# Kernel tuning notes

Measured on AMD Instinct MI355X. Metric: run time of the kernel, lower is better.

The kernel has to match this reference:

```python
import jax, jax.numpy as jnp
import numpy as np

B, T, V, E, H, D = 2048, 50, 65, 100, 20, 5  # batch, block, vocab, n_embd, heads, head_size


def setup_inputs() -> dict:
    key = jax.random.key(0)
    ks = jax.random.split(key, 12)
    idx = jax.random.randint(ks[0], (B, T), 0, V)
    targets = jax.random.randint(ks[1], (B, T), 0, V)
    tok_emb = jax.random.normal(ks[2], (V, E), dtype=jnp.float32) * 0.02
    pos_emb = jax.random.normal(ks[3], (T, E), dtype=jnp.float32) * 0.02
    # per-head Linear(N_EMBD, head_size, bias=False) weights, stacked over heads: [H, D, E]
    Wk = jax.random.normal(ks[4], (H, D, E), dtype=jnp.float32) * 0.1
    Wq = jax.random.normal(ks[5], (H, D, E), dtype=jnp.float32) * 0.1
    Wv = jax.random.normal(ks[6], (H, D, E), dtype=jnp.float32) * 0.1
    W_ff = jax.random.normal(ks[7], (E, E), dtype=jnp.float32) * 0.1
    b_ff = jnp.zeros((E,), dtype=jnp.float32)
    W_lm = jax.random.normal(ks[8], (V, E), dtype=jnp.float32) * 0.1
    b_lm = jnp.zeros((V,), dtype=jnp.float32)
    return {"idx": idx, "targets": targets, "tok_emb": tok_emb, "pos_emb": pos_emb,
            "Wk": Wk, "Wq": Wq, "Wv": Wv, "W_ff": W_ff, "b_ff": b_ff,
            "W_lm": W_lm, "b_lm": b_lm}


def reference(idx, targets, tok_emb, pos_emb, Wk, Wq, Wv, W_ff, b_ff, W_lm, b_lm):
    Bs, Ts = idx.shape
    x = tok_emb[idx] + pos_emb[:Ts]  # [B, T, E]
    # batched over all heads (equivalent to the per-head Python loop + concat)
    k = jnp.einsum('bte,hde->bhtd', x, Wk)
    q = jnp.einsum('bte,hde->bhtd', x, Wq)
    v = jnp.einsum('bte,hde->bhtd', x, Wv)
    # NOTE: faithful to original: k @ q^T, scaled by C**0.5 (multiply, C = N_EMBD)
    scale = jnp.asarray(E, x.dtype) ** 0.5
    w = jnp.einsum('bhtd,bhsd->bhts', k, q) * scale  # [B, H, T, S]
    tril = jnp.tril(jnp.ones((Ts, Ts), dtype=bool))
    w = jnp.where(tril, w, -jnp.inf)
    # original: torch.softmax(weights, dim=1) on [B, T, S] -> axis 't' here (axis=2)
    w = jax.nn.softmax(w, axis=2)
    attn = jnp.einsum('bhts,bhsd->bhtd', w, v)
    attn = attn.transpose(0, 2, 1, 3).reshape(Bs, Ts, H * D)  # concat heads -> [B, T, E]
    h = jax.nn.relu(attn @ W_ff.T + b_ff)  # FeedForward applied AFTER attention
    logits = h @ W_lm.T + b_lm  # [B, T, V]
    logits2d = logits.reshape(Bs * Ts, V)
    tflat = targets.reshape(Bs * Ts)
    logp = jax.nn.log_softmax(logits2d, axis=-1)
    loss = -jnp.take_along_axis(logp, tflat[:, None], axis=-1).mean()
    return (logits2d, loss)
```

## Files before the change

kernel.cpp:

```cpp
#include <hip/hip_runtime.h>
#include <hip/hip_bf16.h>

#define Bb 2048
#define Tt 50
#define Vv 65
#define Ee 100
#define Hh 20
#define Dd 5

typedef __bf16 v8bf __attribute__((ext_vector_type(8)));
typedef short v8s __attribute__((ext_vector_type(8)));
typedef short v4s __attribute__((ext_vector_type(4)));
typedef float f32x4 __attribute__((ext_vector_type(4)));

__device__ __forceinline__ v8bf bzero8() {
    v8s z = {0, 0, 0, 0, 0, 0, 0, 0};
    union { v8s s; v8bf b; } u; u.s = z; return u.b;
}
__device__ __forceinline__ unsigned short bfbits(float f) {
    union { __hip_bfloat16 h; unsigned short s; } c;
    c.h = __float2bfloat16(f);
    return c.s;
}
__device__ __forceinline__ float bf2f(short s) {
    union { unsigned i; float f; } c; c.i = ((unsigned)(unsigned short)s) << 16; return c.f;
}
__device__ __forceinline__ unsigned pack2(float a, float b) {
    return (unsigned)bfbits(a) | ((unsigned)bfbits(b) << 16);
}

__device__ __forceinline__ f32x4 mfma_16x16x16_bf16(v4s a, v4s b, f32x4 c) {
#if __has_builtin(__builtin_amdgcn_mfma_f32_16x16x16bf16_1k)
    return __builtin_amdgcn_mfma_f32_16x16x16bf16_1k(a, b, c, 0, 0, 0);
#else
    f32x4 d;
    asm volatile("v_mfma_f32_16x16x16_bf16 %0, %1, %2, %3\n\ts_nop 7\n\ts_nop 4"
                 : "=v"(d) : "v"(a), "v"(b), "v"(c));
    return d;
#endif
}

#define WS_WKQV 1024
#define WS_WFF  (1024 + 81920)
#define WS_WLM  (1024 + 81920 + 32768)

#define XSTR 136
#define QLO 0
#define QHI 4000
#define KLO 5000
#define KHI 9000
#define R3V 10000
#define HST 6800
#define VSTR 52

__global__ __launch_bounds__(256) void prep_kernel(
    const float* __restrict__ Wk, const float* __restrict__ Wq,
    const float* __restrict__ Wv, const float* __restrict__ Wff,
    const float* __restrict__ Wlm, char* __restrict__ ws,
    float* __restrict__ out)
{
    int g = blockIdx.x * 256 + threadIdx.x;
    if (g == 0) out[Bb * Tt * Vv] = 0.f;
    __hip_bfloat16* wkqv = (__hip_bfloat16*)(ws + WS_WKQV);
    __hip_bfloat16* wff  = (__hip_bfloat16*)(ws + WS_WFF);
    __hip_bfloat16* wlm  = (__hip_bfloat16*)(ws + WS_WLM);
    if (g < 40960) {
        int n = g >> 7, e = g & 127;
        float v = 0.f;
        if (e < Ee) {
            if (n < 100)      v = Wk[n * Ee + e] * 14.4269504089f;
            else if (n < 200) v = Wq[(n - 100) * Ee + e];
            else if (n < 300) v = Wv[(n - 200) * Ee + e];
        }
        wkqv[g] = __float2bfloat16(v);
    } else if (g < 57344) {
        int gg = g - 40960; int n = gg >> 7, e = gg & 127;
        float v = (e < Ee && n < Ee) ? Wff[n * Ee + e] : 0.f;
        wff[gg] = __float2bfloat16(v);
    } else {
        int gg = g - 57344; int n = gg >> 7, e = gg & 127;
        float v = (e < Ee && n < Vv) ? Wlm[n * Ee + e] : 0.f;
        wlm[gg] = __float2bfloat16(v);
    }
}

__global__ __launch_bounds__(256, 4) void gpt_main(
    const int* __restrict__ idx, const int* __restrict__ targets,
    const float* __restrict__ tok_emb, const float* __restrict__ pos_emb,
    const float* __restrict__ b_ff, const float* __restrict__ b_lm,
    const char* __restrict__ ws, float* __restrict__ out)
{
    __shared__ __attribute__((aligned(16))) __hip_bfloat16 sh[15200];
    __shared__ int tok_s[Tt];
    __shared__ float bsum;

    const int b    = blockIdx.x;
    const int tid  = threadIdx.x;
    const int wave = tid >> 6;
    const int ln   = tid & 15;
    const int quad = (tid >> 4) & 3;

    if (tid < Tt) tok_s[tid] = idx[b * Tt + tid];
    if (tid == 0) bsum = 0.f;
    __syncthreads();
    for (int i = tid; i < Tt * 32; i += 256) {
        int r = i >> 5, c4 = (i & 31) * 4;
        ushort4 o;
        if (c4 < Ee) {
            const float4 te = *(const float4*)&tok_emb[tok_s[r] * Ee + c4];
            const float4 pe = *(const float4*)&pos_emb[r * Ee + c4];
            o.x = bfbits(te.x + pe.x); o.y = bfbits(te.y + pe.y);
            o.z = bfbits(te.z + pe.z); o.w = bfbits(te.w + pe.w);
        } else {
            o.x = 0; o.y = 0; o.z = 0; o.w = 0;
        }
        *(ushort4*)&sh[r * XSTR + c4] = o;
    }
    __syncthreads();

    {
        const __hip_bfloat16* wkqv = (const __hip_bfloat16*)(ws + WS_WKQV);
        f32x4 acc[5][4];
#pragma unroll
        for (int j = 0; j < 5; ++j)
#pragma unroll
            for (int mt = 0; mt < 4; ++mt) {
                f32x4 z = {0.f, 0.f, 0.f, 0.f};
                acc[j][mt] = z;
            }
#pragma unroll
        for (int kt = 0; kt < 4; ++kt) {
            v8bf a[4];
#pragma unroll
            for (int mt = 0; mt < 4; ++mt)
                a[mt] = (mt < 3 || ln < 2)
                      ? *(const v8bf*)&sh[(mt * 16 + ln) * XSTR + kt * 32 + quad * 8]
                      : bzero8();
#pragma unroll
            for (int j = 0; j < 5; ++j) {
                int nt = wave * 5 + j;
                v8bf bfr = *(const v8bf*)&wkqv[(nt * 16 + ln) * 128 + kt * 32 + quad * 8];
#pragma unroll
                for (int mt = 0; mt < 4; ++mt)
                    acc[j][mt] = __builtin_amdgcn_mfma_f32_16x16x32_bf16(a[mt], bfr, acc[j][mt], 0, 0, 0);
            }
        }
        __syncthreads();
#pragma unroll
        for (int j = 0; j < 5; ++j) {
            int n = (wave * 5 + j) * 16 + ln;
            if (n < 300) {
                int mat = n / 100;
                int jj  = n - mat * 100;
                int h   = jj / 5, d = jj - (jj / 5) * 5;
                if (mat == 2) {
                    int base = R3V + (h * 5 + d) * VSTR;
#pragma unroll
                    for (int mt = 0; mt < 4; ++mt) {
                        if (mt < 3 || quad == 0) {
                            float v0 = acc[j][mt][0], v1 = acc[j][mt][1];
                            float v2 = acc[j][mt][2], v3 = acc[j][mt][3];
                            if (mt == 3) { v2 = 0.f; v3 = 0.f; }
                            uint2 pk = make_uint2(pack2(v0, v1), pack2(v2, v3));
                            *(uint2*)&sh[base + mt * 16 + quad * 4] = pk;
                        }
                    }
                } else {
                    int lo = (mat == 0) ? KLO : QLO;
                    int hi = (mat == 0) ? KHI : QHI;
                    int rbase = h * 50;
#pragma unroll
                    for (int mt = 0; mt < 4; ++mt)
#pragma unroll
                        for (int r = 0; r < 4; ++r) {
                            int m = mt * 16 + quad * 4 + r;
                            if (m < Tt) {
                                __hip_bfloat16 val = __float2bfloat16(acc[j][mt][r]);
                                if (d < 4) sh[lo + (rbase + m) * 4 + d] = val;
                                else       sh[hi + rbase + m] = val;
                            }
                        }
                }
            }
        }
    }
    __syncthreads();

    unsigned attp[5][8];
    {
        const float BIGF = 3.0e38f;
        float dA1[4], d50[4];
#pragma unroll
        for (int r = 0; r < 4; ++r) {
            int qr = quad * 4 + r;
            dA1[r] = (ln >= qr) ? BIGF : 0.f;
            d50[r] = (qr < 2)  ? BIGF : 0.f;
        }
        const float tl3 = (ln < 2) ? BIGF : 0.f;

#pragma unroll
        for (int hj = 0; hj < 5; ++hj) {
            const int h = wave * 5 + hj;
            v8bf qf[4], kf[4];
#pragma unroll
            for (int i = 0; i < 4; ++i) {
                int row = h * 50 + i * 16 + ln;
                if (quad == 0) {
                    union { unsigned long long u[2]; v8bf b; } uq, uk;
                    uq.u[0] = *(const unsigned long long*)&sh[QLO + row * 4];
                    uq.u[1] = (unsigned long long)*(const unsigned short*)&sh[QHI + row];
                    uk.u[0] = *(const unsigned long long*)&sh[KLO + row * 4];
                    uk.u[1] = (unsigned long long)*(const unsigned short*)&sh[KHI + row];
                    qf[i] = uq.b; kf[i] = uk.b;
                } else {
                    qf[i] = bzero8(); kf[i] = bzero8();
                }
            }
            f32x4 pac[4];
#pragma unroll
            for (int mt = 0; mt < 4; ++mt) { f32x4 z = {0.f, 0.f, 0.f, 0.f}; pac[mt] = z; }
#pragma unroll
            for (int ms = 0; ms < 4; ++ms) {
                float esum[4] = {0.f, 0.f, 0.f, 0.f};
                v4s afs[4];
#pragma unroll
                for (int u = 0; u < 4 - ms; ++u) {
                    f32x4 z = {0.f, 0.f, 0.f, 0.f};
                    f32x4 t1 = __builtin_amdgcn_mfma_f32_16x16x32_bf16(qf[ms], kf[ms + u], z, 0, 0, 0);
                    v4s af;
#pragma unroll
                    for (int r = 0; r < 4; ++r) {
                        float x = __builtin_amdgcn_exp2f(t1[r]);
                        if (u == 0)      x = fminf(x, dA1[r]);
                        if (ms + u == 3) x = fminf(x, tl3);
                        if (ms == 3)     x = fminf(x, d50[r]);
                        esum[r] += x;
                        af[r] = (short)bfbits(x);
                    }
                    afs[u] = af;
                }
#pragma unroll
                for (int r = 0; r < 4; ++r) {
                    float e = esum[r];
                    e += __shfl_xor(e, 1);
                    e += __shfl_xor(e, 2);
                    e += __shfl_xor(e, 4);
                    e += __shfl_xor(e, 8);
                    esum[r] = e;
                }
                float rdv[4];
#pragma unroll
                for (int r = 0; r < 4; ++r)
                    rdv[r] = (ms < 3 || (quad * 4 + r) < 2)
                           ? __builtin_amdgcn_rcpf(esum[r]) : 0.f;
                v4s braw;
                if (ln < Dd && (ms < 3 || quad == 0))
                    braw = *(const v4s*)&sh[R3V + (h * 5 + ln) * VSTR + ms * 16 + quad * 4];
                else { v4s zz = {0, 0, 0, 0}; braw = zz; }
                v4s bvt;
#pragma unroll
                for (int j = 0; j < 4; ++j)
                    bvt[j] = (short)bfbits(bf2f(braw[j]) * rdv[j]);
#pragma unroll
                for (int u = 0; u < 4 - ms; ++u)
                    pac[ms + u] = mfma_16x16x16_bf16(afs[u], bvt, pac[ms + u]);
            }
#pragma unroll
            for (int mt = 0; mt < 4; ++mt) {
                attp[hj][mt * 2]     = pack2(pac[mt][0], pac[mt][1]);
                attp[hj][mt * 2 + 1] = pack2(pac[mt][2], pac[mt][3]);
            }
        }
    }
    __syncthreads();

#pragma unroll
    for (int hj = 0; hj < 5; ++hj) {
        int col = (wave * 5 + hj) * 5 + ln;
#pragma unroll
        for (int mt = 0; mt < 4; ++mt)
#pragma unroll
            for (int r = 0; r < 4; ++r) {
                int t = mt * 16 + quad * 4 + r;
                if (ln < Dd && t < Tt) {
                    unsigned w = attp[hj][mt * 2 + (r >> 1)];
                    unsigned short v = (unsigned short)((r & 1) ? (w >> 16) : (w & 0xffff));
                    *(unsigned short*)&sh[t * XSTR + col] = v;
                }
            }
    }
    __syncthreads();

    {
        const __hip_bfloat16* wff = (const __hip_bfloat16*)(ws + WS_WFF);
        f32x4 fac[2][4];
#pragma unroll
        for (int u = 0; u < 2; ++u)
#pragma unroll
            for (int mt = 0; mt < 4; ++mt) {
                f32x4 z = {0.f, 0.f, 0.f, 0.f};
                fac[u][mt] = z;
            }
        const int nn = (wave < 3) ? 2 : 1;
#pragma unroll
        for (int kt = 0; kt < 4; ++kt) {
            v8bf a[4];
#pragma unroll
            for (int mt = 0; mt < 4; ++mt)
                a[mt] = (mt < 3 || ln < 2)
                      ? *(const v8bf*)&sh[(mt * 16 + ln) * XSTR + kt * 32 + quad * 8]
                      : bzero8();
#pragma unroll
            for (int u = 0; u < 2; ++u) {
                if (u < nn) {
                    int nt = wave + u * 4;
                    v8bf bfr = *(const v8bf*)&wff[(nt * 16 + ln) * 128 + kt * 32 + quad * 8];
#pragma unroll
                    for (int mt = 0; mt < 4; ++mt)
                        fac[u][mt] = __builtin_amdgcn_mfma_f32_16x16x32_bf16(a[mt], bfr, fac[u][mt], 0, 0, 0);
                }
            }
        }
#pragma unroll
        for (int u = 0; u < 2; ++u) {
            if (u < nn) {
                int n = (wave + u * 4) * 16 + ln;
                if (n < Ee) {
                    float bias = b_ff[n];
#pragma unroll
                    for (int mt = 0; mt < 4; ++mt)
#pragma unroll
                        for (int r = 0; r < 4; ++r) {
                            int m = mt * 16 + quad * 4 + r;
                            if (m < Tt) {
                                float v = fac[u][mt][r] + bias;
                                sh[HST + m * XSTR + n] = __float2bfloat16(v > 0.f ? v : 0.f);
                            }
                        }
                }
            }
        }
    }
    __syncthreads();

    {
        const __hip_bfloat16* wlm = (const __hip_bfloat16*)(ws + WS_WLM);
        float* lgl = (float*)sh;
#pragma unroll
        for (int i = 0; i < 5; ++i) {
            int job = wave + i * 4;
            int mt = job / 5, nt = job - (job / 5) * 5;
            f32x4 acc = {0.f, 0.f, 0.f, 0.f};
#pragma unroll
            for (int kt = 0; kt < 4; ++kt) {
                v8bf a = (mt < 3 || ln < 2)
                       ? *(const v8bf*)&sh[HST + (mt * 16 + ln) * XSTR + kt * 32 + quad * 8]
                       : bzero8();
                v8bf bf = *(const v8bf*)&wlm[(nt * 16 + ln) * 128 + kt * 32 + quad * 8];
                acc = __builtin_amdgcn_mfma_f32_16x16x32_bf16(a, bf, acc, 0, 0, 0);
            }
            int n = nt * 16 + ln;
            if (n < Vv) {
                float bias = b_lm[n];
#pragma unroll
                for (int r = 0; r < 4; ++r) {
                    int m = mt * 16 + quad * 4 + r;
                    if (m < Tt) {
                        float v = acc[r] + bias;
                        out[(b * Tt + m) * Vv + n] = v;
                        lgl[m * 68 + n] = v;
                    }
                }
            }
        }
    }
    __syncthreads();

    if (tid < 200) {
        int r = tid >> 2, lv = tid & 3;
        const float* row = (const float*)sh + r * 68;
        float mx = -3.0e38f;
        for (int v = lv; v < Vv; v += 4) mx = fmaxf(mx, row[v]);
        mx = fmaxf(mx, __shfl_xor(mx, 1));
        mx = fmaxf(mx, __shfl_xor(mx, 2));
        float sum = 0.f;
        for (int v = lv; v < Vv; v += 4)
            sum += __builtin_amdgcn_exp2f((row[v] - mx) * 1.4426950408889634f);
        sum += __shfl_xor(sum, 1);
        sum += __shfl_xor(sum, 2);
        if (lv == 0) {
            float lse = mx + 0.69314718055994531f * log2f(sum);
            int tgt = targets[b * Tt + r];
            atomicAdd(&bsum, lse - row[tgt]);
        }
    }
    __syncthreads();
    if (tid == 0)
        atomicAdd(&out[Bb * Tt * Vv], bsum * (1.0f / (float)(Bb * Tt)));
}

extern "C" void kernel_launch(void* const* d_in, const int* in_sizes, int n_in,
                              void* d_out, int out_size, void* d_ws, size_t ws_size,
                              hipStream_t stream)
{
    const int* idx     = (const int*)d_in[0];
    const int* targets = (const int*)d_in[1];
    const float* tok_emb = (const float*)d_in[2];
    const float* pos_emb = (const float*)d_in[3];
    const float* Wk  = (const float*)d_in[4];
    const float* Wq  = (const float*)d_in[5];
    const float* Wv  = (const float*)d_in[6];
    const float* Wff = (const float*)d_in[7];
    const float* bff = (const float*)d_in[8];
    const float* Wlm = (const float*)d_in[9];
    const float* blm = (const float*)d_in[10];
    float* out = (float*)d_out;
    char* ws = (char*)d_ws;

    hipLaunchKernelGGL(prep_kernel, dim3(264), dim3(256), 0, stream, Wk, Wq, Wv, Wff, Wlm, ws, out);
    hipLaunchKernelGGL(gpt_main, dim3(Bb), dim3(256), 0, stream,
                       idx, targets, tok_emb, pos_emb, bff, blm, (const char*)ws, out);
}
```

Baseline: 193.3 us.

## Compute softmax column sums via MFMA and store attention output in-place transposed

The per-row exp sums are now computed in a separate MFMA pass over the transposed score tile and reduced across lanes with a multiply by a ones vector, replacing the shuffle-based reduction. Q is stored in a padded 8-wide layout so it loads as one vector. The attention output is written directly over the V buffer in transposed form, which removes the register staging array and one barrier. The feedforward A-operand is then gathered element by element from that transposed layout. The cost is recomputing the score MFMAs and exponentials twice, scalar strided LDS gathers in the FF stage, and a larger shared-memory footprint that may lower occupancy.

```diff
diff --git a/kernel.cpp b/kernel.cpp
--- a/kernel.cpp
+++ b/kernel.cpp
@@ -45,12 +45,10 @@
 #define WS_WLM  (1024 + 81920 + 32768)
 
 #define XSTR 136
-#define QLO 0
-#define QHI 4000
-#define KLO 5000
-#define KHI 9000
-#define R3V 10000
-#define HST 6800
+#define R3V 8000
+#define KLO 13200
+#define KHI 17200
+#define HST 13200
 #define VSTR 52
 
 __global__ __launch_bounds__(256) void prep_kernel(
@@ -90,7 +88,7 @@
     const float* __restrict__ b_ff, const float* __restrict__ b_lm,
     const char* __restrict__ ws, float* __restrict__ out)
 {
-    __shared__ __attribute__((aligned(16))) __hip_bfloat16 sh[15200];
+    __shared__ __attribute__((aligned(16))) __hip_bfloat16 sh[20000];
     __shared__ int tok_s[Tt];
     __shared__ float bsum;
 
@@ -102,6 +100,10 @@
 
     if (tid < Tt) tok_s[tid] = idx[b * Tt + tid];
     if (tid == 0) bsum = 0.f;
+    {
+        const uint4 z4 = make_uint4(0u, 0u, 0u, 0u);
+        for (int i = tid; i < 225; i += 256) ((uint4*)&sh[18200])[i] = z4;
+    }
     __syncthreads();
     for (int i = tid; i < Tt * 32; i += 256) {
         int r = i >> 5, c4 = (i & 31) * 4;
@@ -146,6 +148,10 @@
             }
         }
         __syncthreads();
+        for (int i = tid; i < 1000; i += 256) {
+            *(unsigned short*)&sh[i * 8 + 5] = 0;
+            *(unsigned*)&sh[i * 8 + 6] = 0;
+        }
 #pragma unroll
         for (int j = 0; j < 5; ++j) {
             int n = (wave * 5 + j) * 16 + ln;
@@ -165,9 +171,17 @@
                             *(uint2*)&sh[base + mt * 16 + quad * 4] = pk;
                         }
                     }
+                } else if (mat == 1) {
+                    int rbase = h * 50;
+#pragma unroll
+                    for (int mt = 0; mt < 4; ++mt)
+#pragma unroll
+                        for (int r = 0; r < 4; ++r) {
+                            int m = mt * 16 + quad * 4 + r;
+                            if (m < Tt)
+                                sh[(rbase + m) * 8 + d] = __float2bfloat16(acc[j][mt][r]);
+                        }
                 } else {
-                    int lo = (mat == 0) ? KLO : QLO;
-                    int hi = (mat == 0) ? KHI : QHI;
                     int rbase = h * 50;
 #pragma unroll
                     for (int mt = 0; mt < 4; ++mt)
@@ -176,8 +190,8 @@
                             int m = mt * 16 + quad * 4 + r;
                             if (m < Tt) {
                                 __hip_bfloat16 val = __float2bfloat16(acc[j][mt][r]);
-                                if (d < 4) sh[lo + (rbase + m) * 4 + d] = val;
-                                else       sh[hi + rbase + m] = val;
+                                if (d < 4) sh[KLO + (rbase + m) * 4 + d] = val;
+                                else       sh[KHI + rbase + m] = val;
                             }
                         }
                 }
@@ -186,17 +200,19 @@
     }
     __syncthreads();
 
-    unsigned attp[5][8];
     {
         const float BIGF = 3.0e38f;
-        float dA1[4], d50[4];
+        float dA2[4], dA1[4], d50[4];
 #pragma unroll
         for (int r = 0; r < 4; ++r) {
             int qr = quad * 4 + r;
+            dA2[r] = (qr >= ln) ? BIGF : 0.f;
             dA1[r] = (ln >= qr) ? BIGF : 0.f;
             d50[r] = (qr < 2)  ? BIGF : 0.f;
         }
         const float tl3 = (ln < 2) ? BIGF : 0.f;
+
+        v4s ones4; ones4[0] = ones4[1] = ones4[2] = ones4[3] = (short)0x3F80;
 
 #pragma unroll
         for (int hj = 0; hj < 5; ++hj) {
@@ -206,12 +222,11 @@
             for (int i = 0; i < 4; ++i) {
                 int row = h * 50 + i * 16 + ln;
                 if (quad == 0) {
-                    union { unsigned long long u[2]; v8bf b; } uq, uk;
-                    uq.u[0] = *(const unsigned long long*)&sh[QLO + row * 4];
-                    uq.u[1] = (unsigned long long)*(const unsigned short*)&sh[QHI + row];
+                    qf[i] = *(const v8bf*)&sh[row * 8];
+                    union { unsigned long long u[2]; v8bf b; } uk;
                     uk.u[0] = *(const unsigned long long*)&sh[KLO + row * 4];
                     uk.u[1] = (unsigned long long)*(const unsigned short*)&sh[KHI + row];
-                    qf[i] = uq.b; kf[i] = uk.b;
+                    kf[i] = uk.b;
                 } else {
                     qf[i] = bzero8(); kf[i] = bzero8();
                 }
@@ -222,7 +237,36 @@
 #pragma unroll
             for (int ms = 0; ms < 4; ++ms) {
                 float esum[4] = {0.f, 0.f, 0.f, 0.f};
-                v4s afs[4];
+#pragma unroll
+                for (int mt = ms; mt < 4; ++mt) {
+                    f32x4 z = {0.f, 0.f, 0.f, 0.f};
+                    f32x4 t2 = __builtin_amdgcn_mfma_f32_16x16x32_bf16(kf[mt], qf[ms], z, 0, 0, 0);
+#pragma unroll
+                    for (int r = 0; r < 4; ++r) {
+                        float x = __builtin_amdgcn_exp2f(t2[r]);
+                        if (mt == ms) x = fminf(x, dA2[r]);
+                        if (mt == 3)  x = fminf(x, d50[r]);
+                        esum[r] += x;
+                    }
+                }
+                v4s af0;
+                af0[0] = (short)bfbits(esum[0]); af0[1] = (short)bfbits(esum[1]);
+                af0[2] = (short)bfbits(esum[2]); af0[3] = (short)bfbits(esum[3]);
+                f32x4 z0 = {0.f, 0.f, 0.f, 0.f};
+                f32x4 dres = mfma_16x16x16_bf16(af0, ones4, z0);
+                float rdv[4];
+#pragma unroll
+                for (int r = 0; r < 4; ++r)
+                    rdv[r] = (ms < 3 || (quad * 4 + r) < 2)
+                           ? __builtin_amdgcn_rcpf(dres[r]) : 0.f;
+                v4s braw;
+                if (ln < Dd && (ms < 3 || quad == 0))
+                    braw = *(const v4s*)&sh[R3V + (h * 5 + ln) * VSTR + ms * 16 + quad * 4];
+                else { v4s zz = {0, 0, 0, 0}; braw = zz; }
+                v4s bvt;
+#pragma unroll
+                for (int j = 0; j < 4; ++j)
+                    bvt[j] = (short)bfbits(bf2f(braw[j]) * rdv[j]);
 #pragma unroll
                 for (int u = 0; u < 4 - ms; ++u) {
                     f32x4 z = {0.f, 0.f, 0.f, 0.f};
@@ -234,60 +278,22 @@
                         if (u == 0)      x = fminf(x, dA1[r]);
                         if (ms + u == 3) x = fminf(x, tl3);
                         if (ms == 3)     x = fminf(x, d50[r]);
-                        esum[r] += x;
                         af[r] = (short)bfbits(x);
                     }
-                    afs[u] = af;
-                }
-#pragma unroll
-                for (int r = 0; r < 4; ++r) {
-                    float e = esum[r];
-                    e += __shfl_xor(e, 1);
-                    e += __shfl_xor(e, 2);
-                    e += __shfl_xor(e, 4);
-                    e += __shfl_xor(e, 8);
-                    esum[r] = e;
-                }
-                float rdv[4];
-#pragma unroll
-                for (int r = 0; r < 4; ++r)
-                    rdv[r] = (ms < 3 || (quad * 4 + r) < 2)
-                           ? __builtin_amdgcn_rcpf(esum[r]) : 0.f;
-                v4s braw;
-                if (ln < Dd && (ms < 3 || quad == 0))
-                    braw = *(const v4s*)&sh[R3V + (h * 5 + ln) * VSTR + ms * 16 + quad * 4];
-                else { v4s zz = {0, 0, 0, 0}; braw = zz; }
-                v4s bvt;
-#pragma unroll
-                for (int j = 0; j < 4; ++j)
-                    bvt[j] = (short)bfbits(bf2f(braw[j]) * rdv[j]);
-#pragma unroll
-                for (int u = 0; u < 4 - ms; ++u)
-                    pac[ms + u] = mfma_16x16x16_bf16(afs[u], bvt, pac[ms + u]);
-            }
-#pragma unroll
-            for (int mt = 0; mt < 4; ++mt) {
-                attp[hj][mt * 2]     = pack2(pac[mt][0], pac[mt][1]);
-                attp[hj][mt * 2 + 1] = pack2(pac[mt][2], pac[mt][3]);
-            }
-        }
-    }
-    __syncthreads();
-
-#pragma unroll
-    for (int hj = 0; hj < 5; ++hj) {
-        int col = (wave * 5 + hj) * 5 + ln;
-#pragma unroll
-        for (int mt = 0; mt < 4; ++mt)
-#pragma unroll
-            for (int r = 0; r < 4; ++r) {
-                int t = mt * 16 + quad * 4 + r;
-                if (ln < Dd && t < Tt) {
-                    unsigned w = attp[hj][mt * 2 + (r >> 1)];
-                    unsigned short v = (unsigned short)((r & 1) ? (w >> 16) : (w & 0xffff));
-                    *(unsigned short*)&sh[t * XSTR + col] = v;
-                }
-            }
+                    pac[ms + u] = mfma_16x16x16_bf16(af, bvt, pac[ms + u]);
+                }
+            }
+            if (ln < Dd) {
+                int base = R3V + (h * 5 + ln) * VSTR;
+#pragma unroll
+                for (int mt = 0; mt < 3; ++mt) {
+                    *(unsigned*)&sh[base + mt * 16 + quad * 4]     = pack2(pac[mt][0], pac[mt][1]);
+                    *(unsigned*)&sh[base + mt * 16 + quad * 4 + 2] = pack2(pac[mt][2], pac[mt][3]);
+                }
+                if (quad == 0)
+                    *(unsigned*)&sh[base + 48] = pack2(pac[3][0], pac[3][1]);
+            }
+        }
     }
     __syncthreads();
 
@@ -306,10 +312,20 @@
         for (int kt = 0; kt < 4; ++kt) {
             v8bf a[4];
 #pragma unroll
-            for (int mt = 0; mt < 4; ++mt)
-                a[mt] = (mt < 3 || ln < 2)
-                      ? *(const v8bf*)&sh[(mt * 16 + ln) * XSTR + kt * 32 + quad * 8]
-                      : bzero8();
+            for (int mt = 0; mt < 4; ++mt) {
+                const int m = mt * 16 + ln;
+                const bool rowok = (mt < 3) || (ln < 2);
+                const int c0 = kt * 32 + quad * 8;
+                union { unsigned short u[8]; v8bf b; } ua;
+#pragma unroll
+                for (int e = 0; e < 8; ++e) {
+                    int c = c0 + e;
+                    ua.u[e] = (rowok && c < Ee)
+                            ? *(const unsigned short*)&sh[R3V + c * VSTR + m]
+                            : (unsigned short)0;
+                }
+                a[mt] = ua.b;
+            }
 #pragma unroll
             for (int u = 0; u < 2; ++u) {
                 if (u < nn) {
```

New measurement: 188.1 us. 1.03x faster.
